# Kernel optimization log

Hardware: AMD Instinct MI355X
Metric: run time of the kernel (lower is better)

## Reference

```python
import jax, jax.numpy as jnp
import numpy as np

DT = 1e-3
TAU_SYN_INV = 200.0      # 1/5e-3
TAU_MEM_INV = 100.0      # 1/1e-2
TAU_ADAPT_INV = 1.0 / 700.0
V_TH = 1.0
BETA = 1.8
ALPHA = 100.0            # SuperSpike surrogate slope
SEQ_LEN = 40
SCALE = 50.0


@jax.custom_vjp
def superspike(x):
    return (x > 0).astype(x.dtype)

def _ss_fwd(x):
    return (x > 0).astype(x.dtype), x

def _ss_bwd(x, g):
    # SuperSpike surrogate gradient: 1 / (alpha*|x| + 1)^2
    return (g / (ALPHA * jnp.abs(x) + 1.0) ** 2,)

superspike.defvjp(_ss_fwd, _ss_bwd)


def lif_encode(current):
    """Constant-current LIF encoder: current [B,F] -> spikes [T,B,F]."""
    def step(v, _):
        v = v + DT * TAU_MEM_INV * (-v + current)   # v_leak = 0
        z = superspike(v - V_TH)
        v = (1.0 - z) * v                           # reset to v_reset = 0
        return v, z
    _, spikes = jax.lax.scan(step, jnp.zeros_like(current), None, length=SEQ_LEN)
    return spikes


def setup_inputs() -> dict:
    key = jax.random.key(0)
    kx, k1, k2, k3, kd = jax.random.split(key, 5)
    B, S, H, O = 16384, 4, 128, 2
    x = jax.random.normal(kx, (B, S), jnp.float32)
    w_in = jax.random.normal(k1, (H, 2 * S), jnp.float32) * np.sqrt(2.0 / H).astype(np.float32)
    w_rec = jax.random.normal(k2, (H, H), jnp.float32) * np.sqrt(2.0 / H).astype(np.float32)
    w_out = jax.random.normal(k3, (O, H), jnp.float32) * np.sqrt(2.0 / O).astype(np.float32)
    keep = jax.random.bernoulli(kd, 0.5, (SEQ_LEN, B, H))
    drop_mask = keep.astype(jnp.float32) * 2.0      # inverted dropout, p=0.5
    return {"x": x, "w_in": w_in, "w_rec": w_rec, "w_out": w_out,
            "drop_mask": drop_mask}


def reference(x, w_in, w_rec, w_out, drop_mask):
    # Encode state into pos/neg spike trains: [T, B, 2*S]
    x_pos = lif_encode(jax.nn.relu(SCALE * x))
    x_neg = lif_encode(jax.nn.relu(-SCALE * x))
    inp = jnp.concatenate([x_pos, x_neg], axis=2)

    B = x.shape[0]
    H = w_in.shape[0]
    O = w_out.shape[0]
    zH = jnp.zeros((B, H), x.dtype)
    zO = jnp.zeros((B, O), x.dtype)
    carry0 = (zH, zH, zH, zH, zO, zO)  # (z, v, i, b, v_out, i_out)

    def step(carry, xs):
        z, v, i, b, vo, io = carry
        x_t, m_t = xs
        # --- LSNN cell (norse lsnn_step) ---
        v_dec = v + DT * TAU_MEM_INV * (-v + i)        # v_leak = 0
        i_dec = i - DT * TAU_SYN_INV * i
        b_dec = b + DT * TAU_ADAPT_INV * (V_TH - b)
        z_new = superspike(v_dec - b_dec)
        v_new = (1.0 - z_new) * v_dec                  # v_reset = 0
        i_new = i_dec + x_t @ w_in.T + z @ w_rec.T
        b_new = b_dec + z_new * (TAU_ADAPT_INV * BETA)
        # dropout (training mode, p=0.5, precomputed inverted mask)
        z_d = z_new * m_t
        # --- LI readout (norse li_step) ---
        vo_new = vo + DT * TAU_MEM_INV * (-vo + io)
        io_new = io - DT * TAU_SYN_INV * io + z_d @ w_out.T
        return (z_new, v_new, i_new, b_new, vo_new, io_new), vo_new

    _, voltages = jax.lax.scan(step, carry0, (inp, drop_mask))  # [T, B, O]
    m = jnp.max(voltages, axis=0)
    return jax.nn.softmax(m, axis=1)
```

## Files before the change

### kernel.cpp

```cpp
#include <hip/hip_runtime.h>
#include <math.h>
#include <string.h>

#define TSTEPS 40
#define BTOT   16384
#define HDIM   128
#define BT     64
#define ZSTR   168
#define NWAVE  8
#define NRT    4

typedef __attribute__((ext_vector_type(8))) short bf16x8;
typedef __attribute__((ext_vector_type(4))) float f32x4;
typedef __attribute__((ext_vector_type(4))) unsigned int u32x4;

__device__ __forceinline__ short f2bf(float f) {
    unsigned int u; memcpy(&u, &f, 4);
    u += 0x7fffu + ((u >> 16) & 1u);
    return (short)(u >> 16);
}
__device__ __forceinline__ float bf2f(short s) {
    unsigned int u = ((unsigned int)(unsigned short)s) << 16;
    float f; memcpy(&f, &u, 4);
    return f;
}

__global__ __launch_bounds__(512, 2)
void lsnn9(const float* __restrict__ x,
           const float* __restrict__ w_in,
           const float* __restrict__ w_rec,
           const float* __restrict__ w_out,
           const float* __restrict__ dm,
           float* __restrict__ out)
{
    __shared__ short zbuf[2][BT][ZSTR];
    __shared__ unsigned short maskb[TSTEPS][BT][NWAVE];
    float* sbuf = (float*)&zbuf[0][0][0];

    const int tid   = threadIdx.x;
    const int l     = tid & 63;
    const int wv    = tid >> 6;
    const int li    = l & 15;
    const int q     = l >> 4;
    const int bbase = blockIdx.x * BT;
    const int hcol  = wv * 16 + li;

    bf16x8 wB[5][3];
    #pragma unroll
    for (int kt = 0; kt < 4; ++kt) {
        const float* src = w_rec + hcol * HDIM + kt * 32 + q * 8;
        #pragma unroll
        for (int i = 0; i < 8; ++i) {
            float w0 = src[i];
            short h0 = f2bf(w0); float r1 = w0 - bf2f(h0);
            short h1 = f2bf(r1); float r2 = r1 - bf2f(h1);
            wB[kt][0][i] = h0; wB[kt][1][i] = h1; wB[kt][2][i] = f2bf(r2);
        }
    }
    #pragma unroll
    for (int i = 0; i < 8; ++i) { wB[4][0][i] = 0; wB[4][1][i] = 0; wB[4][2][i] = 0; }
    if (q == 0) {
        const float* src = w_in + hcol * 8;
        #pragma unroll
        for (int i = 0; i < 8; ++i) {
            float w0 = src[i];
            short h0 = f2bf(w0); float r1 = w0 - bf2f(h0);
            short h1 = f2bf(r1); float r2 = r1 - bf2f(h1);
            wB[4][0][i] = h0; wB[4][1][i] = h1; wB[4][2][i] = f2bf(r2);
        }
    }

    f32x4 v[NRT], cu[NRT], ba[NRT];
    #pragma unroll
    for (int rt = 0; rt < NRT; ++rt) {
        v[rt]  = (f32x4){0.f,0.f,0.f,0.f};
        cu[rt] = (f32x4){0.f,0.f,0.f,0.f};
        ba[rt] = (f32x4){0.f,0.f,0.f,0.f};
    }

    const int er = tid >> 3, ech = tid & 7;
    float ve = 0.f, ce;
    {
        float xv = 50.f * x[(bbase + er) * 4 + (ech & 3)];
        ce = (ech < 4) ? fmaxf(xv, 0.f) : fmaxf(-xv, 0.f);
    }

    const float KA = 1.4285714285714286e-06f;
    const float KB = 2.5714285714285714e-03f;

    for (int idx = tid; idx < 2 * BT * ZSTR; idx += 512) ((short*)zbuf)[idx] = 0;
    __syncthreads();

    {
        float vv = ve + 0.1f * (ce - ve);
        float sp = (vv - 1.0f > 0.f) ? 1.f : 0.f;
        ve = (1.f - sp) * vv;
        zbuf[0][er][128 + ech] = (sp > 0.5f) ? (short)0x3F80 : (short)0;
    }

    float fP[16];
    {
        const float* g = dm + (size_t)bbase * HDIM;
        #pragma unroll
        for (int j = 0; j < 16; ++j)
            fP[j] = g[((j >> 2) * 16 + q * 4 + (j & 3)) * HDIM + hcol];
    }

    for (int t = 0; t < TSTEPS; ++t) {
        const int p = t & 1;
        __syncthreads();

        unsigned kb = 0;
        #pragma unroll
        for (int j = 0; j < 16; ++j) kb |= (fP[j] > 1.0f ? 1u : 0u) << j;

        {
            int tn = (t + 1 < TSTEPS) ? t + 1 : TSTEPS - 1;
            const float* g = dm + ((size_t)tn * BTOT + bbase) * HDIM;
            #pragma unroll
            for (int j = 0; j < 16; ++j)
                fP[j] = g[((j >> 2) * 16 + q * 4 + (j & 3)) * HDIM + hcol];
        }

        {
            float vv = ve + 0.1f * (ce - ve);
            float sp = (vv - 1.0f > 0.f) ? 1.f : 0.f;
            ve = (1.f - sp) * vv;
            zbuf[1 - p][er][128 + ech] = (sp > 0.5f) ? (short)0x3F80 : (short)0;
        }

        f32x4 acc[NRT];
        #pragma unroll
        for (int rt = 0; rt < NRT; ++rt) {
            f32x4 a = {0.f, 0.f, 0.f, 0.f};
            #pragma unroll
            for (int kt = 0; kt < 5; ++kt) {
                bf16x8 zA = *reinterpret_cast<const bf16x8*>(&zbuf[p][rt * 16 + li][kt * 32 + q * 8]);
                #pragma unroll
                for (int pp = 0; pp < 3; ++pp)
                    a = __builtin_amdgcn_mfma_f32_16x16x32_bf16(zA, wB[kt][pp], a, 0, 0, 0);
            }
            acc[rt] = a;
        }

        #pragma unroll
        for (int rt = 0; rt < NRT; ++rt) {
            #pragma unroll
            for (int r = 0; r < 4; ++r) {
                const int row = rt * 16 + q * 4 + r;
                float vd = v[rt][r] + 0.1f * (cu[rt][r] - v[rt][r]);
                float id = cu[rt][r] - 0.2f * cu[rt][r];
                float bd = ba[rt][r] + KA * (1.0f - ba[rt][r]);
                float z  = (vd - bd > 0.f) ? 1.f : 0.f;
                v[rt][r]  = (1.f - z) * vd;
                ba[rt][r] = bd + z * KB;
                cu[rt][r] = id + acc[rt][r];
                zbuf[1 - p][row][hcol] = (z > 0.5f) ? (short)0x3F80 : (short)0;
                unsigned long long bm = __ballot((z > 0.5f) && ((kb >> (rt * 4 + r)) & 1u));
                if (li == 0)
                    maskb[t][row][wv] = (unsigned short)(bm >> (q * 16));
            }
        }
    }

    __syncthreads();
    asm volatile("" ::: "memory");

    bf16x8 woB[4][2];
    #pragma unroll
    for (int kt = 0; kt < 4; ++kt) {
        #pragma unroll
        for (int i = 0; i < 8; ++i) {
            float w0 = 0.f;
            if (li < 2) w0 = w_out[li * HDIM + kt * 32 + q * 8 + i];
            short h0 = f2bf(w0);
            woB[kt][0][i] = h0;
            woB[kt][1][i] = f2bf(w0 - bf2f(h0));
        }
    }
    for (int T = wv; T < TSTEPS * NRT; T += NWAVE) {
        const int t  = T >> 2;
        const int rt = T & 3;
        f32x4 ac = {0.f, 0.f, 0.f, 0.f};
        #pragma unroll
        for (int kt = 0; kt < 4; ++kt) {
            unsigned b = (unsigned)maskb[t][rt * 16 + li][2 * kt + (q >> 1)];
            b = (b >> ((q & 1) * 8)) & 0xffu;
            u32x4 aw;
            aw.x = ((b & 1u)   << 14) | ((b & 2u)   << 29);
            aw.y = ((b & 4u)   << 12) | ((b & 8u)   << 27);
            aw.z = ((b & 16u)  << 10) | ((b & 32u)  << 25);
            aw.w = ((b & 64u)  <<  8) | ((b & 128u) << 23);
            bf16x8 A = __builtin_bit_cast(bf16x8, aw);
            ac = __builtin_amdgcn_mfma_f32_16x16x32_bf16(A, woB[kt][0], ac, 0, 0, 0);
            ac = __builtin_amdgcn_mfma_f32_16x16x32_bf16(A, woB[kt][1], ac, 0, 0, 0);
        }
        if (li < 2) {
            #pragma unroll
            for (int r = 0; r < 4; ++r)
                sbuf[((size_t)t * BT + rt * 16 + q * 4 + r) * 2 + li] = ac[r];
        }
    }
    __syncthreads();

    if (wv < 2) {
        const int g = wv * 64 + l;
        const int row = g >> 1, o = g & 1;
        float vo = 0.f, io = 0.f, mx = 0.f;
        for (int t = 0; t < TSTEPS; ++t) {
            float s = sbuf[((size_t)t * BT + row) * 2 + o];
            float von = vo + 0.1f * (io - vo);
            io = io - 0.2f * io + s;
            vo = von;
            mx = fmaxf(mx, vo);
        }
        float other = __shfl_xor(mx, 1);
        float mmax  = fmaxf(mx, other);
        float e  = expf(mx - mmax);
        float eo = expf(other - mmax);
        out[(size_t)(bbase + row) * 2 + o] = e / (e + eo);
    }
}

extern "C" void kernel_launch(void* const* d_in, const int* in_sizes, int n_in,
                              void* d_out, int out_size, void* d_ws, size_t ws_size,
                              hipStream_t stream) {
    const float* x     = (const float*)d_in[0];
    const float* w_in  = (const float*)d_in[1];
    const float* w_rec = (const float*)d_in[2];
    const float* w_out = (const float*)d_in[3];
    const float* dmask = (const float*)d_in[4];
    float* outp = (float*)d_out;

    lsnn9<<<BTOT / BT, 512, 0, stream>>>(x, w_in, w_rec, w_out, dmask, outp);
}
```

Measured before the change: 462.1 us.

## Split recurrence and dropout-mask readout into two kernels via workspace

Splits the kernel in two. The first kernel runs the recurrent LSNN scan without reading the dropout mask and writes the raw spike bitmasks to global workspace. The second kernel streams the large dropout mask with double-buffered loads, ANDs it into the spike bits, then runs the readout MFMA and softmax. The goal is to take the 335MB mask stream off the latency-bound serial recurrence so it can be read at full bandwidth. The cost is an extra launch and a workspace round trip of the bitmasks.

After: 552.6 us. +19.6%, slower.

```diff
diff --git a/kernel.cpp b/kernel.cpp
--- a/kernel.cpp
+++ b/kernel.cpp
@@ -9,6 +9,7 @@
 #define ZSTR   168
 #define NWAVE  8
 #define NRT    4
+#define MB_U16 (TSTEPS * BT * NWAVE)
 
 typedef __attribute__((ext_vector_type(8))) short bf16x8;
 typedef __attribute__((ext_vector_type(4))) float f32x4;
@@ -26,16 +27,13 @@
 }
 
 __global__ __launch_bounds__(512, 2)
-void lsnn9(const float* __restrict__ x,
+void lsnnA(const float* __restrict__ x,
            const float* __restrict__ w_in,
            const float* __restrict__ w_rec,
-           const float* __restrict__ w_out,
-           const float* __restrict__ dm,
-           float* __restrict__ out)
+           unsigned short* __restrict__ gmask)
 {
     __shared__ short zbuf[2][BT][ZSTR];
     __shared__ unsigned short maskb[TSTEPS][BT][NWAVE];
-    float* sbuf = (float*)&zbuf[0][0][0];
 
     const int tid   = threadIdx.x;
     const int l     = tid & 63;
@@ -98,29 +96,9 @@
         zbuf[0][er][128 + ech] = (sp > 0.5f) ? (short)0x3F80 : (short)0;
     }
 
-    float fP[16];
-    {
-        const float* g = dm + (size_t)bbase * HDIM;
-        #pragma unroll
-        for (int j = 0; j < 16; ++j)
-            fP[j] = g[((j >> 2) * 16 + q * 4 + (j & 3)) * HDIM + hcol];
-    }
-
     for (int t = 0; t < TSTEPS; ++t) {
         const int p = t & 1;
         __syncthreads();
-
-        unsigned kb = 0;
-        #pragma unroll
-        for (int j = 0; j < 16; ++j) kb |= (fP[j] > 1.0f ? 1u : 0u) << j;
-
-        {
-            int tn = (t + 1 < TSTEPS) ? t + 1 : TSTEPS - 1;
-            const float* g = dm + ((size_t)tn * BTOT + bbase) * HDIM;
-            #pragma unroll
-            for (int j = 0; j < 16; ++j)
-                fP[j] = g[((j >> 2) * 16 + q * 4 + (j & 3)) * HDIM + hcol];
-        }
 
         {
             float vv = ve + 0.1f * (ce - ve);
@@ -156,7 +134,7 @@
                 ba[rt][r] = bd + z * KB;
                 cu[rt][r] = id + acc[rt][r];
                 zbuf[1 - p][row][hcol] = (z > 0.5f) ? (short)0x3F80 : (short)0;
-                unsigned long long bm = __ballot((z > 0.5f) && ((kb >> (rt * 4 + r)) & 1u));
+                unsigned long long bm = __ballot(z > 0.5f);
                 if (li == 0)
                     maskb[t][row][wv] = (unsigned short)(bm >> (q * 16));
             }
@@ -164,7 +142,29 @@
     }
 
     __syncthreads();
-    asm volatile("" ::: "memory");
+    {
+        u32x4* dst = (u32x4*)(gmask + (size_t)blockIdx.x * MB_U16);
+        const u32x4* src = (const u32x4*)&maskb[0][0][0];
+        for (int i = tid; i < MB_U16 / 8; i += 512) dst[i] = src[i];
+    }
+}
+
+__global__ __launch_bounds__(512, 2)
+void lsnnB(const float* __restrict__ dm,
+           const float* __restrict__ w_out,
+           const unsigned short* __restrict__ gmask,
+           float* __restrict__ out)
+{
+    __shared__ unsigned short mb[TSTEPS][BT][NWAVE];
+    __shared__ float sbuf[TSTEPS][BT][2];
+
+    const int tid   = threadIdx.x;
+    const int l     = tid & 63;
+    const int wv    = tid >> 6;
+    const int li    = l & 15;
+    const int q     = l >> 4;
+    const int bbase = blockIdx.x * BT;
+    const int hcol  = wv * 16 + li;
 
     bf16x8 woB[4][2];
     #pragma unroll
@@ -178,13 +178,53 @@
             woB[kt][1][i] = f2bf(w0 - bf2f(h0));
         }
     }
+
+    {
+        const u32x4* src = (const u32x4*)(gmask + (size_t)blockIdx.x * MB_U16);
+        u32x4* dst = (u32x4*)&mb[0][0][0];
+        for (int i = tid; i < MB_U16 / 8; i += 512) dst[i] = src[i];
+    }
+    __syncthreads();
+
+    float bk0[16], bk1[16];
+#define LOADT(tt, bk)                                                          \
+    {                                                                          \
+        const float* g = dm + ((size_t)(tt) * BTOT + bbase) * HDIM;            \
+        _Pragma("unroll")                                                      \
+        for (int j = 0; j < 16; ++j)                                           \
+            bk[j] = g[((j >> 2) * 16 + q * 4 + (j & 3)) * HDIM + hcol];        \
+    }
+#define USET(tt, bk)                                                           \
+    {                                                                          \
+        _Pragma("unroll")                                                      \
+        for (int j = 0; j < 16; ++j) {                                         \
+            unsigned long long bm = __ballot(bk[j] > 1.0f);                    \
+            if (li == 0) {                                                     \
+                const int row = (j >> 2) * 16 + q * 4 + (j & 3);               \
+                mb[tt][row][wv] &= (unsigned short)(bm >> (q * 16));           \
+            }                                                                  \
+        }                                                                      \
+    }
+    LOADT(0, bk0)
+    LOADT(1, bk1)
+    #pragma unroll 4
+    for (int tt = 0; tt < TSTEPS; tt += 2) {
+        USET(tt, bk0)
+        { int tn = (tt + 2 < TSTEPS) ? tt + 2 : TSTEPS - 1; LOADT(tn, bk0) }
+        USET(tt + 1, bk1)
+        { int tn = (tt + 3 < TSTEPS) ? tt + 3 : TSTEPS - 1; LOADT(tn, bk1) }
+    }
+#undef LOADT
+#undef USET
+    __syncthreads();
+
     for (int T = wv; T < TSTEPS * NRT; T += NWAVE) {
         const int t  = T >> 2;
         const int rt = T & 3;
         f32x4 ac = {0.f, 0.f, 0.f, 0.f};
         #pragma unroll
         for (int kt = 0; kt < 4; ++kt) {
-            unsigned b = (unsigned)maskb[t][rt * 16 + li][2 * kt + (q >> 1)];
+            unsigned b = (unsigned)mb[t][rt * 16 + li][2 * kt + (q >> 1)];
             b = (b >> ((q & 1) * 8)) & 0xffu;
             u32x4 aw;
             aw.x = ((b & 1u)   << 14) | ((b & 2u)   << 29);
@@ -198,7 +238,7 @@
         if (li < 2) {
             #pragma unroll
             for (int r = 0; r < 4; ++r)
-                sbuf[((size_t)t * BT + rt * 16 + q * 4 + r) * 2 + li] = ac[r];
+                sbuf[t][rt * 16 + q * 4 + r][li] = ac[r];
         }
     }
     __syncthreads();
@@ -208,7 +248,7 @@
         const int row = g >> 1, o = g & 1;
         float vo = 0.f, io = 0.f, mx = 0.f;
         for (int t = 0; t < TSTEPS; ++t) {
-            float s = sbuf[((size_t)t * BT + row) * 2 + o];
+            float s = sbuf[t][row][o];
             float von = vo + 0.1f * (io - vo);
             io = io - 0.2f * io + s;
             vo = von;
@@ -231,6 +271,8 @@
     const float* w_out = (const float*)d_in[3];
     const float* dmask = (const float*)d_in[4];
     float* outp = (float*)d_out;
-
-    lsnn9<<<BTOT / BT, 512, 0, stream>>>(x, w_in, w_rec, w_out, dmask, outp);
-}
+    unsigned short* gm = (unsigned short*)d_ws;
+
+    lsnnA<<<BTOT / BT, 512, 0, stream>>>(x, w_in, w_rec, gm);
+    lsnnB<<<BTOT / BT, 512, 0, stream>>>(dmask, w_out, gm, outp);
+}
```
